# Kernel tuning notes

Measured on AMD Instinct MI355X. Metric: run time of the kernel, lower is better.

The kernel has to match this reference:

```python
import jax, jax.numpy as jnp
from jax import lax
import numpy as np

N, T, U = 8, 300, 60
E_ENC, E_DEC, NHID, VOCAB, BLANK = 320, 320, 512, 128, 0


def setup_inputs() -> dict:
    key = jax.random.key(0)
    ks = jax.random.split(key, 6)
    enc_state = jax.random.normal(ks[0], (N, T, E_ENC), jnp.float32)
    dec_state = jax.random.normal(ks[1], (N, U + 1, E_DEC), jnp.float32)
    targets = jax.random.randint(ks[2], (N, U), 1, VOCAB, jnp.int32)  # non-blank labels
    inputs_len = jnp.full((N,), T, jnp.int32)
    targets_len = jnp.full((N,), U, jnp.int32)
    W_joint = jax.random.normal(ks[3], (E_ENC + E_DEC, NHID), jnp.float32) * (1.0 / np.sqrt(E_ENC + E_DEC))
    b_joint = jnp.zeros((NHID,), jnp.float32)
    W_out = jax.random.normal(ks[4], (NHID, VOCAB), jnp.float32) * (1.0 / np.sqrt(NHID))
    b_out = jnp.zeros((VOCAB,), jnp.float32)
    return dict(enc_state=enc_state, dec_state=dec_state, targets=targets,
                inputs_len=inputs_len, targets_len=targets_len,
                W_joint=W_joint, b_joint=b_joint, W_out=W_out, b_out=b_out)


def _joint_log_probs(enc, dec, Wj, bj, Wo, bo):
    # Original: broadcast enc [N,T,1,Ee] + dec [N,1,U1,Ed], concat, Linear, Tanh, Linear, log_softmax.
    # Splitting W_joint over the concat axis is exactly equivalent and avoids the [N,T,U1,Ee+Ed] tensor.
    Ee = enc.shape[-1]
    h = (jnp.einsum('nte,eh->nth', enc, Wj[:Ee])[:, :, None, :]
         + jnp.einsum('nue,eh->nuh', dec, Wj[Ee:])[:, None, :, :]
         + bj)                                              # [N,T,U1,NHID]
    logits = jnp.einsum('ntuh,hv->ntuv', jnp.tanh(h), Wo) + bo  # [N,T,U1,V]
    return jax.nn.log_softmax(logits, axis=-1)


def _rnnt_loss(logp, targets, inputs_len, targets_len, blank):
    # Forward (alpha) DP over the T x (U+1) lattice, vectorized over batch.
    Nb, Tt, U1, V = logp.shape
    blank_lp = logp[..., blank]                                        # [N,T,U1]
    emit_lp = jnp.take_along_axis(logp[:, :, :U1 - 1, :],
                                  targets[:, None, :, None], axis=-1)[..., 0]  # [N,T,U]
    # Row t=0: alpha[0,u] = sum_{u'<u} emit[0,u'].
    a0 = jnp.concatenate([jnp.zeros((Nb, 1), logp.dtype),
                          jnp.cumsum(emit_lp[:, 0, :], axis=1)], axis=1)       # [N,U1]

    def row_step(prev, xs):
        blank_tm1, emit_t = xs                      # [N,U1], [N,U]
        base = prev + blank_tm1                     # path arriving from (t-1,u) via blank

        def u_step(carry, xs_u):
            b_u, e_u = xs_u                         # [N], [N]
            v = jnp.logaddexp(b_u, carry + e_u)     # blank-from-below vs emit-from-left
            return v, v

        _, rest = lax.scan(u_step, base[:, 0], (base[:, 1:].T, emit_t.T))      # [U,N]
        row = jnp.concatenate([base[:, :1], rest.T], axis=1)                   # [N,U1]
        return row, row

    _, rows = lax.scan(row_step, a0,
                       (jnp.swapaxes(blank_lp[:, :-1], 0, 1),
                        jnp.swapaxes(emit_lp[:, 1:], 0, 1)))                   # [T-1,N,U1]
    alpha = jnp.concatenate([a0[:, None, :], jnp.swapaxes(rows, 0, 1)], axis=1)  # [N,T,U1]

    ti = (inputs_len - 1).astype(jnp.int32)
    ui = targets_len.astype(jnp.int32)
    n = jnp.arange(Nb)
    log_p = alpha[n, ti, ui] + blank_lp[n, ti, ui]  # final blank transition
    return -log_p


def reference(enc_state, dec_state, targets, inputs_len, targets_len,
              W_joint, b_joint, W_out, b_out):
    logp = _joint_log_probs(enc_state, dec_state, W_joint, b_joint, W_out, b_out)
    loss = _rnnt_loss(logp, targets, inputs_len, targets_len, BLANK)
    return loss.mean()
```

## Files before the change

kernel.cpp:

```cpp
#include <hip/hip_runtime.h>
#include <hip/hip_bf16.h>
#include <hip/hip_fp16.h>

#define N_   8
#define T_   300
#define U_   60
#define U1_  61
#define EENC 320
#define NHID 512
#define VOC  128
#define SKROWS 384
#define INV_LN2 1.4426950408889634f
#define LN2 0.6931471805599453f
#define SCALE2 2.8853900817779268f

typedef __attribute__((ext_vector_type(8))) short bf16x8;
typedef __attribute__((ext_vector_type(4))) float f32x4;

__device__ __forceinline__ unsigned short f2bf(float f) {
    unsigned int u = __float_as_uint(f);
    u += 0x7fff + ((u >> 16) & 1);
    return (unsigned short)(u >> 16);
}

__device__ __forceinline__ float lae2(float x, float y) {
    float m = fmaxf(x, y);
    float d = fminf(fabsf(x - y), 1e30f);
    return m + log2f(1.f + exp2f(-d));
}

__device__ __forceinline__ unsigned gload4(const void* p) {
    unsigned v;
    asm volatile("global_load_dword %0, %1, off" : "=v"(v) : "v"(p) : "memory");
    return v;
}

__global__ __launch_bounds__(256) void convert_w(
    const float* __restrict__ Wj, const float* __restrict__ Wo,
    unsigned short* __restrict__ WjT, unsigned short* __restrict__ WoT2,
    float* __restrict__ bosum)
{
    __shared__ float tile[32][33];
    int bid = blockIdx.x;
    const float* S; unsigned short* D; int k0, c0, K, C; bool isWo;
    if (bid < 160) { S = Wj; D = WjT; K = 320; C = 512; k0 = (bid >> 4) * 32; c0 = (bid & 15) * 32; isWo = false; }
    else { bid -= 160; S = Wo; D = WoT2; K = 512; C = 128; k0 = (bid >> 2) * 32; c0 = (bid & 3) * 32; isWo = true; }
    const int tx = threadIdx.x & 31, ty = threadIdx.x >> 5;
    float part = 0.f;
    #pragma unroll
    for (int i = 0; i < 32; i += 8) {
        float v = S[(k0 + ty + i) * C + c0 + tx];
        tile[ty + i][tx] = v;
        part += v;
    }
    __syncthreads();
    const float mulf = isWo ? -2.f : 1.f;
    #pragma unroll
    for (int i = 0; i < 32; i += 8)
        D[(c0 + ty + i) * K + k0 + tx] = f2bf(mulf * tile[tx][ty + i]);
    if (isWo) atomicAdd(&bosum[c0 + tx], part);
}

__global__ __launch_bounds__(256) void proj_mfma(
    const float* __restrict__ Xe, const float* __restrict__ Xd,
    const unsigned short* __restrict__ BT,
    const float* __restrict__ bj,
    float* __restrict__ Ce, float* __restrict__ Cd)
{
    __shared__ short lA[64 * 64];
    __shared__ short lB[128 * 64];
    int bid = blockIdx.x;
    const float* X; float* Cp; const float* bias; int R;
    if (bid < 152) { X = Xe; Cp = Ce; bias = nullptr; R = N_ * T_; }
    else { bid -= 152; X = Xd; Cp = Cd; bias = bj; R = N_ * U1_; }
    const int tid = threadIdx.x, lane = tid & 63, wave = tid >> 6;
    const int rb = bid >> 2, cb = bid & 3;
    const int rh = wave & 1, ch = wave >> 1;
    const int sr = tid >> 3, sg = tid & 7;
    const int frow = lane & 15, fg = lane >> 4, quad = lane >> 4;

    f32x4 acc[2][4];
    f32x4 z = {0.f, 0.f, 0.f, 0.f};
    #pragma unroll
    for (int a = 0; a < 2; ++a)
        #pragma unroll
        for (int b = 0; b < 4; ++b) acc[a][b] = z;

    for (int s = 0; s < 5; ++s) {
        __syncthreads();
        #pragma unroll
        for (int p = 0; p < 2; ++p) {
            int row = sr + p * 32;
            int grow = rb * 64 + row; if (grow >= R) grow = R - 1;
            const float* xp = X + grow * EENC + s * 64 + sg * 8;
            float4 x0 = *(const float4*)xp, x1 = *(const float4*)(xp + 4);
            bf16x8 va;
            va[0] = (short)f2bf(x0.x); va[1] = (short)f2bf(x0.y);
            va[2] = (short)f2bf(x0.z); va[3] = (short)f2bf(x0.w);
            va[4] = (short)f2bf(x1.x); va[5] = (short)f2bf(x1.y);
            va[6] = (short)f2bf(x1.z); va[7] = (short)f2bf(x1.w);
            *(bf16x8*)&lA[row * 64 + ((sg ^ (row & 7)) << 3)] = va;
        }
        #pragma unroll
        for (int p = 0; p < 4; ++p) {
            int col = sr + p * 32;
            bf16x8 vb = *(const bf16x8*)(BT + (cb * 128 + col) * EENC + s * 64 + sg * 8);
            *(bf16x8*)&lB[col * 64 + ((sg ^ (col & 7)) << 3)] = vb;
        }
        __syncthreads();
        #pragma unroll
        for (int ks = 0; ks < 2; ++ks) {
            int g = fg + ks * 4;
            bf16x8 af[2], bf[4];
            #pragma unroll
            for (int rt = 0; rt < 2; ++rt) {
                int row = rh * 32 + rt * 16 + frow;
                af[rt] = *(const bf16x8*)&lA[row * 64 + ((g ^ (row & 7)) << 3)];
            }
            #pragma unroll
            for (int c = 0; c < 4; ++c) {
                int col = ch * 64 + c * 16 + frow;
                bf[c] = *(const bf16x8*)&lB[col * 64 + ((g ^ (col & 7)) << 3)];
            }
            #pragma unroll
            for (int rt = 0; rt < 2; ++rt)
                #pragma unroll
                for (int c = 0; c < 4; ++c)
                    acc[rt][c] = __builtin_amdgcn_mfma_f32_16x16x32_bf16(af[rt], bf[c], acc[rt][c], 0, 0, 0);
        }
    }
    #pragma unroll
    for (int rt = 0; rt < 2; ++rt) {
        int grow0 = rb * 64 + rh * 32 + rt * 16 + quad * 4;
        #pragma unroll
        for (int c = 0; c < 4; ++c) {
            int col = cb * 128 + ch * 64 + c * 16 + frow;
            float b = bias ? bias[col] : 0.f;
            #pragma unroll
            for (int r = 0; r < 4; ++r) {
                int gr = grow0 + r;
                if (gr < R)
                    Cp[gr * NHID + col] = __builtin_amdgcn_exp2f((acc[rt][c][r] + b) * SCALE2);
            }
        }
    }
}

__device__ __forceinline__ void sigstore(short* lAp, float4 ee0, float4 ee1,
                                         float4 dd0, float4 dd1, int row, int sg)
{
    float s0 = __builtin_amdgcn_rcpf(__builtin_fmaf(ee0.x, dd0.x, 1.f));
    float s1 = __builtin_amdgcn_rcpf(__builtin_fmaf(ee0.y, dd0.y, 1.f));
    float s2 = __builtin_amdgcn_rcpf(__builtin_fmaf(ee0.z, dd0.z, 1.f));
    float s3 = __builtin_amdgcn_rcpf(__builtin_fmaf(ee0.w, dd0.w, 1.f));
    float s4 = __builtin_amdgcn_rcpf(__builtin_fmaf(ee1.x, dd1.x, 1.f));
    float s5 = __builtin_amdgcn_rcpf(__builtin_fmaf(ee1.y, dd1.y, 1.f));
    float s6 = __builtin_amdgcn_rcpf(__builtin_fmaf(ee1.z, dd1.z, 1.f));
    float s7 = __builtin_amdgcn_rcpf(__builtin_fmaf(ee1.w, dd1.w, 1.f));
    unsigned b0 = __float_as_uint(s0) + 0x8000u, b1 = __float_as_uint(s1) + 0x8000u;
    unsigned b2 = __float_as_uint(s2) + 0x8000u, b3 = __float_as_uint(s3) + 0x8000u;
    unsigned b4 = __float_as_uint(s4) + 0x8000u, b5 = __float_as_uint(s5) + 0x8000u;
    unsigned b6 = __float_as_uint(s6) + 0x8000u, b7 = __float_as_uint(s7) + 0x8000u;
    union { unsigned u4[4]; bf16x8 v; } va;
    va.u4[0] = __builtin_amdgcn_perm(b1, b0, 0x07060302);
    va.u4[1] = __builtin_amdgcn_perm(b3, b2, 0x07060302);
    va.u4[2] = __builtin_amdgcn_perm(b5, b4, 0x07060302);
    va.u4[3] = __builtin_amdgcn_perm(b7, b6, 0x07060302);
    *(bf16x8*)&lAp[row * 64 + ((sg ^ (row & 7)) << 3)] = va.v;
}

__global__ __launch_bounds__(256, 5) void joint_mfma(
    const float* __restrict__ encp,
    const float* __restrict__ decp,
    const unsigned short* __restrict__ WoT2,
    const float* __restrict__ bo, const float* __restrict__ bosum,
    const int* __restrict__ targets,
    unsigned short* __restrict__ Zs)
{
    __shared__ short lA[64 * 64];
    __shared__ short lB[128 * 64];
    __shared__ float bo_s[VOC];
    __shared__ int   lab_s[U_];

    const int tid = threadIdx.x, lane = tid & 63, wave = tid >> 6;
    const int nt = blockIdx.x;
    const int n = nt / T_, t0 = nt - n * T_;
    if (tid < VOC) bo_s[tid] = bo[tid] + bosum[tid];
    else if (tid < VOC + U_) lab_s[tid - VOC] = targets[n * U_ + (tid - VOC)];

    const int frow = lane & 15, quad = lane >> 4;
    const int sg = tid & 7, sr = tid >> 3;

    f32x4 acc[8];
    f32x4 z = {0.f, 0.f, 0.f, 0.f};
    #pragma unroll
    for (int c = 0; c < 8; ++c) acc[c] = z;

    const int ua0 = min(sr, U_);
    const int ua1 = min(sr + 32, U_);
    const float* dbase0 = decp + (size_t)(n * U1_ + ua0) * NHID + sg * 8;
    const float* dbase1 = decp + (size_t)(n * U1_ + ua1) * NHID + sg * 8;
    const float* ebase  = encp + (size_t)nt * NHID + sg * 8;
    const unsigned short* wbase = WoT2 + sg * 8;

    float4 e0, e1, d00, d01, d10, d11;
    bf16x8 vb0, vb1, vb2, vb3;
    e0  = *(const float4*)ebase;        e1  = *(const float4*)(ebase + 4);
    d00 = *(const float4*)dbase0;       d01 = *(const float4*)(dbase0 + 4);
    d10 = *(const float4*)dbase1;       d11 = *(const float4*)(dbase1 + 4);
    vb0 = *(const bf16x8*)(wbase + (size_t)(sr +  0) * NHID);
    vb1 = *(const bf16x8*)(wbase + (size_t)(sr + 32) * NHID);
    vb2 = *(const bf16x8*)(wbase + (size_t)(sr + 64) * NHID);
    vb3 = *(const bf16x8*)(wbase + (size_t)(sr + 96) * NHID);

    for (int s = 0; s < 8; ++s) {
        __syncthreads();
        { int col = sr;      *(bf16x8*)&lB[col * 64 + ((sg ^ (col & 7)) << 3)] = vb0; }
        { int col = sr + 32; *(bf16x8*)&lB[col * 64 + ((sg ^ (col & 7)) << 3)] = vb1; }
        { int col = sr + 64; *(bf16x8*)&lB[col * 64 + ((sg ^ (col & 7)) << 3)] = vb2; }
        { int col = sr + 96; *(bf16x8*)&lB[col * 64 + ((sg ^ (col & 7)) << 3)] = vb3; }
        sigstore(lA, e0, e1, d00, d01, sr,      sg);
        sigstore(lA, e0, e1, d10, d11, sr + 32, sg);
        __syncthreads();
        if (s < 7) {
            const int o = (s + 1) * 64;
            e0  = *(const float4*)(ebase + o);      e1  = *(const float4*)(ebase + o + 4);
            d00 = *(const float4*)(dbase0 + o);     d01 = *(const float4*)(dbase0 + o + 4);
            d10 = *(const float4*)(dbase1 + o);     d11 = *(const float4*)(dbase1 + o + 4);
            vb0 = *(const bf16x8*)(wbase + (size_t)(sr +  0) * NHID + o);
            vb1 = *(const bf16x8*)(wbase + (size_t)(sr + 32) * NHID + o);
            vb2 = *(const bf16x8*)(wbase + (size_t)(sr + 64) * NHID + o);
            vb3 = *(const bf16x8*)(wbase + (size_t)(sr + 96) * NHID + o);
        }
        __builtin_amdgcn_s_setprio(1);
        #pragma unroll
        for (int ks = 0; ks < 2; ++ks) {
            const int g = ks * 4 + quad;
            int ar = wave * 16 + frow;
            bf16x8 af = *(const bf16x8*)&lA[ar * 64 + ((g ^ (ar & 7)) << 3)];
            #pragma unroll
            for (int c = 0; c < 8; ++c) {
                int col = c * 16 + frow;
                const bf16x8 bfr = *(const bf16x8*)&lB[col * 64 + ((g ^ (col & 7)) << 3)];
                acc[c] = __builtin_amdgcn_mfma_f32_16x16x32_bf16(af, bfr, acc[c], 0, 0, 0);
            }
        }
        __builtin_amdgcn_s_setprio(0);
    }

    #pragma unroll
    for (int c = 0; c < 8; ++c) {
        float b = bo_s[c * 16 + frow];
        #pragma unroll
        for (int r = 0; r < 4; ++r) acc[c][r] += b;
    }
    float mx[4], sm[4];
    #pragma unroll
    for (int r = 0; r < 4; ++r) {
        float m = acc[0][r];
        #pragma unroll
        for (int c = 1; c < 8; ++c) m = fmaxf(m, acc[c][r]);
        mx[r] = m;
    }
    #pragma unroll
    for (int off = 1; off < 16; off <<= 1)
        #pragma unroll
        for (int r = 0; r < 4; ++r) mx[r] = fmaxf(mx[r], __shfl_xor(mx[r], off));
    #pragma unroll
    for (int r = 0; r < 4; ++r) {
        float ss = 0.f;
        #pragma unroll
        for (int c = 0; c < 8; ++c) ss += __expf(acc[c][r] - mx[r]);
        sm[r] = ss;
    }
    #pragma unroll
    for (int off = 1; off < 16; off <<= 1)
        #pragma unroll
        for (int r = 0; r < 4; ++r) sm[r] += __shfl_xor(sm[r], off);

    #pragma unroll
    for (int r = 0; r < 4; ++r) {
        float lse = mx[r] + __logf(sm[r]);
        int urow = wave * 16 + quad * 4 + r;
        size_t rowz = (size_t)(n * SKROWS + t0 + urow + 1) * 64;
        if (urow < U1_ && frow == 0) {
            __half hh = __float2half_rn((acc[0][r] - lse) * INV_LN2);
            Zs[(rowz + urow) * 2] = __half_as_ushort(hh);
        }
        if (urow < U_) {
            int lab = lab_s[urow];
            if (frow == (lab & 15)) {
                int cw = lab >> 4;
                float pick = acc[0][r];
                #pragma unroll
                for (int c = 1; c < 8; ++c) if (c == cw) pick = acc[c][r];
                __half hh = __float2half_rn((pick - lse) * INV_LN2);
                Zs[(rowz + urow + 1) * 2 + 1] = __half_as_ushort(hh);
            }
        }
    }
}

__global__ __launch_bounds__(512) void dp_kernel(
    const unsigned* __restrict__ Z,
    const int* __restrict__ inputs_len, const int* __restrict__ targets_len,
    float* __restrict__ out)
{
    __shared__ float losses[N_];
    const int tid = threadIdx.x;
    const int n = tid >> 6;
    const int u = tid & 63;
    const bool u_is0 = (u == 0);

    const unsigned len_t = (unsigned)inputs_len[n];
    const int ui = targets_len[n];
    const int ti = (int)len_t - 1;

    const char* Zn = (const char*)(Z + (size_t)n * SKROWS * 64) + u * 4;

    float a = u_is0 ? 0.f : -1e30f;

    unsigned zq[16];
    #pragma unroll
    for (int j = 0; j < 16; ++j) zq[j] = gload4(Zn + (size_t)(1 + j) * 256);

    for (int d0 = 1; d0 < 361; d0 += 16) {
        const char* pn = Zn + (size_t)(d0 + 16) * 256;
        #pragma unroll
        for (int j = 0; j < 16; ++j) {
            const int d = d0 + j;
            asm volatile("s_waitcnt vmcnt(15)");
            asm volatile("" : "+v"(zq[j]));
            unsigned zv = zq[j];
            zq[j] = gload4(pn + (size_t)j * 256);
            union { unsigned u32; __half2 h2; } cv; cv.u32 = zv;
            float2 w = __half22float2(cv.h2);
            float av = __shfl_up(a, 1);
            float b  = a + w.x;
            float e  = av + (u_is0 ? -1e30f : w.y);
            float nn = lae2(b, e);
            a = ((unsigned)(d - u) < len_t) ? nn : a;
        }
    }

    if (u == ui) {
        const unsigned* Zb = Z + (size_t)n * SKROWS * 64;
        unsigned wf = Zb[(size_t)(ti + ui + 1) * 64 + ui];
        union { unsigned u32; __half2 h2; } cf; cf.u32 = wf;
        float blf = __half22float2(cf.h2).x;
        losses[n] = -(a + blf) * LN2;
    }
    __syncthreads();
    if (tid == 0) {
        float s = 0.f;
        #pragma unroll
        for (int i = 0; i < N_; ++i) s += losses[i];
        out[0] = s * (1.0f / N_);
    }
}

extern "C" void kernel_launch(void* const* d_in, const int* in_sizes, int n_in,
                              void* d_out, int out_size, void* d_ws, size_t ws_size,
                              hipStream_t stream)
{
    const float* enc         = (const float*)d_in[0];
    const float* dec         = (const float*)d_in[1];
    const int*   targets     = (const int*)d_in[2];
    const int*   inputs_len  = (const int*)d_in[3];
    const int*   targets_len = (const int*)d_in[4];
    const float* Wj          = (const float*)d_in[5];
    const float* bj          = (const float*)d_in[6];
    const float* Wo          = (const float*)d_in[7];
    const float* bo          = (const float*)d_in[8];
    float* out = (float*)d_out;

    char* ws = (char*)d_ws;
    float*          encp  = (float*)(ws + 0);
    float*          decp  = (float*)(ws + 4915200);
    unsigned*       Z     = (unsigned*)(ws + 5914624);
    unsigned short* WjT   = (unsigned short*)(ws + 6701056);
    unsigned short* WoT2  = (unsigned short*)(ws + 7028736);
    float*          bosum = (float*)(ws + 7159872);

    hipMemsetAsync(bosum, 0, VOC * sizeof(float), stream);
    convert_w<<<224, 256, 0, stream>>>(Wj, Wo, WjT, WoT2, bosum);
    proj_mfma<<<184, 256, 0, stream>>>(enc, dec, WjT, bj, encp, decp);
    joint_mfma<<<2400, 256, 0, stream>>>(encp, decp, WoT2, bo, bosum, targets, (unsigned short*)Z);
    dp_kernel<<<1, 512, 0, stream>>>(Z, inputs_len, targets_len, out);
}
```

Baseline: 184.6 us.

## Process two time steps per joint block to share W_out and decoder tiles

Each joint_mfma block now covers two consecutive (n,t) rows with 512 threads and 8 waves, keeping two A tiles in LDS while loading the B tile of W_out and the decoder projections only once. This halves the global loads of W_out and decoder data per time step and halves the block count. The cost is larger blocks with more LDS per block, fewer blocks per CU, and pairs of t that must not straddle a batch boundary (T=300 is even, so they do not).

```diff
diff --git a/kernel.cpp b/kernel.cpp
--- a/kernel.cpp
+++ b/kernel.cpp
@@ -169,7 +169,7 @@
     *(bf16x8*)&lAp[row * 64 + ((sg ^ (row & 7)) << 3)] = va.v;
 }
 
-__global__ __launch_bounds__(256, 5) void joint_mfma(
+__global__ __launch_bounds__(512, 4) void joint_mfma(
     const float* __restrict__ encp,
     const float* __restrict__ decp,
     const unsigned short* __restrict__ WoT2,
@@ -177,67 +177,63 @@
     const int* __restrict__ targets,
     unsigned short* __restrict__ Zs)
 {
-    __shared__ short lA[64 * 64];
+    __shared__ short lA[2][64 * 64];
     __shared__ short lB[128 * 64];
     __shared__ float bo_s[VOC];
     __shared__ int   lab_s[U_];
 
     const int tid = threadIdx.x, lane = tid & 63, wave = tid >> 6;
-    const int nt = blockIdx.x;
-    const int n = nt / T_, t0 = nt - n * T_;
+    const int nt0 = 2 * blockIdx.x;
+    const int n = nt0 / T_, t0 = nt0 - n * T_;
     if (tid < VOC) bo_s[tid] = bo[tid] + bosum[tid];
     else if (tid < VOC + U_) lab_s[tid - VOC] = targets[n * U_ + (tid - VOC)];
 
     const int frow = lane & 15, quad = lane >> 4;
     const int sg = tid & 7, sr = tid >> 3;
+    const int wnt = wave >> 2;
+    const int wr  = wave & 3;
 
     f32x4 acc[8];
     f32x4 z = {0.f, 0.f, 0.f, 0.f};
     #pragma unroll
     for (int c = 0; c < 8; ++c) acc[c] = z;
 
-    const int ua0 = min(sr, U_);
-    const int ua1 = min(sr + 32, U_);
-    const float* dbase0 = decp + (size_t)(n * U1_ + ua0) * NHID + sg * 8;
-    const float* dbase1 = decp + (size_t)(n * U1_ + ua1) * NHID + sg * 8;
-    const float* ebase  = encp + (size_t)nt * NHID + sg * 8;
+    const int ua = min(sr, U_);
+    const float* dbase  = decp + (size_t)(n * U1_ + ua) * NHID + sg * 8;
+    const float* ebase0 = encp + (size_t)nt0 * NHID + sg * 8;
+    const float* ebase1 = ebase0 + NHID;
     const unsigned short* wbase = WoT2 + sg * 8;
 
-    float4 e0, e1, d00, d01, d10, d11;
-    bf16x8 vb0, vb1, vb2, vb3;
-    e0  = *(const float4*)ebase;        e1  = *(const float4*)(ebase + 4);
-    d00 = *(const float4*)dbase0;       d01 = *(const float4*)(dbase0 + 4);
-    d10 = *(const float4*)dbase1;       d11 = *(const float4*)(dbase1 + 4);
+    float4 e0, e1, f0, f1, d0, d1;
+    bf16x8 vb0, vb1;
+    e0 = *(const float4*)ebase0;        e1 = *(const float4*)(ebase0 + 4);
+    f0 = *(const float4*)ebase1;        f1 = *(const float4*)(ebase1 + 4);
+    d0 = *(const float4*)dbase;         d1 = *(const float4*)(dbase + 4);
     vb0 = *(const bf16x8*)(wbase + (size_t)(sr +  0) * NHID);
-    vb1 = *(const bf16x8*)(wbase + (size_t)(sr + 32) * NHID);
-    vb2 = *(const bf16x8*)(wbase + (size_t)(sr + 64) * NHID);
-    vb3 = *(const bf16x8*)(wbase + (size_t)(sr + 96) * NHID);
+    vb1 = *(const bf16x8*)(wbase + (size_t)(sr + 64) * NHID);
 
     for (int s = 0; s < 8; ++s) {
         __syncthreads();
         { int col = sr;      *(bf16x8*)&lB[col * 64 + ((sg ^ (col & 7)) << 3)] = vb0; }
-        { int col = sr + 32; *(bf16x8*)&lB[col * 64 + ((sg ^ (col & 7)) << 3)] = vb1; }
-        { int col = sr + 64; *(bf16x8*)&lB[col * 64 + ((sg ^ (col & 7)) << 3)] = vb2; }
-        { int col = sr + 96; *(bf16x8*)&lB[col * 64 + ((sg ^ (col & 7)) << 3)] = vb3; }
-        sigstore(lA, e0, e1, d00, d01, sr,      sg);
-        sigstore(lA, e0, e1, d10, d11, sr + 32, sg);
+        { int col = sr + 64; *(bf16x8*)&lB[col * 64 + ((sg ^ (col & 7)) << 3)] = vb1; }
+        sigstore(lA[0], e0, e1, d0, d1, sr, sg);
+        sigstore(lA[1], f0, f1, d0, d1, sr, sg);
         __syncthreads();
         if (s < 7) {
             const int o = (s + 1) * 64;
-            e0  = *(const float4*)(ebase + o);      e1  = *(const float4*)(ebase + o + 4);
-            d00 = *(const float4*)(dbase0 + o);     d01 = *(const float4*)(dbase0 + o + 4);
-            d10 = *(const float4*)(dbase1 + o);     d11 = *(const float4*)(dbase1 + o + 4);
+            e0 = *(const float4*)(ebase0 + o);      e1 = *(const float4*)(ebase0 + o + 4);
+            f0 = *(const float4*)(ebase1 + o);      f1 = *(const float4*)(ebase1 + o + 4);
+            d0 = *(const float4*)(dbase + o);       d1 = *(const float4*)(dbase + o + 4);
             vb0 = *(const bf16x8*)(wbase + (size_t)(sr +  0) * NHID + o);
-            vb1 = *(const bf16x8*)(wbase + (size_t)(sr + 32) * NHID + o);
-            vb2 = *(const bf16x8*)(wbase + (size_t)(sr + 64) * NHID + o);
-            vb3 = *(const bf16x8*)(wbase + (size_t)(sr + 96) * NHID + o);
-        }
+            vb1 = *(const bf16x8*)(wbase + (size_t)(sr + 64) * NHID + o);
+        }
+        const short* lAp = lA[wnt];
         __builtin_amdgcn_s_setprio(1);
         #pragma unroll
         for (int ks = 0; ks < 2; ++ks) {
             const int g = ks * 4 + quad;
-            int ar = wave * 16 + frow;
-            bf16x8 af = *(const bf16x8*)&lA[ar * 64 + ((g ^ (ar & 7)) << 3)];
+            int ar = wr * 16 + frow;
+            bf16x8 af = *(const bf16x8*)&lAp[ar * 64 + ((g ^ (ar & 7)) << 3)];
             #pragma unroll
             for (int c = 0; c < 8; ++c) {
                 int col = c * 16 + frow;
@@ -278,11 +274,12 @@
         #pragma unroll
         for (int r = 0; r < 4; ++r) sm[r] += __shfl_xor(sm[r], off);
 
+    const int myt = t0 + wnt;
     #pragma unroll
     for (int r = 0; r < 4; ++r) {
         float lse = mx[r] + __logf(sm[r]);
-        int urow = wave * 16 + quad * 4 + r;
-        size_t rowz = (size_t)(n * SKROWS + t0 + urow + 1) * 64;
+        int urow = wr * 16 + quad * 4 + r;
+        size_t rowz = (size_t)(n * SKROWS + myt + urow + 1) * 64;
         if (urow < U1_ && frow == 0) {
             __half hh = __float2half_rn((acc[0][r] - lse) * INV_LN2);
             Zs[(rowz + urow) * 2] = __half_as_ushort(hh);
@@ -385,6 +382,6 @@
     hipMemsetAsync(bosum, 0, VOC * sizeof(float), stream);
     convert_w<<<224, 256, 0, stream>>>(Wj, Wo, WjT, WoT2, bosum);
     proj_mfma<<<184, 256, 0, stream>>>(enc, dec, WjT, bj, encp, decp);
-    joint_mfma<<<2400, 256, 0, stream>>>(encp, decp, WoT2, bo, bosum, targets, (unsigned short*)Z);
+    joint_mfma<<<1200, 512, 0, stream>>>(encp, decp, WoT2, bo, bosum, targets, (unsigned short*)Z);
     dp_kernel<<<1, 512, 0, stream>>>(Z, inputs_len, targets_len, out);
 }
```

Result: faster. 179.3 us, median of 2 (-2.9%).
